# Kernel tuning notes

Hardware: AMD Instinct MI355X
Metric: run time of the kernel (lower is better)

## Reference

```python
import jax, jax.numpy as jnp
import numpy as np

EPS = 1e-8
ACT_BITS = 8


def _ternary_vq(t):
    gamma = jnp.abs(t).mean()
    q = jnp.clip(jnp.round(t / (gamma + EPS)), -1.0, 1.0)
    return q * gamma


def setup_inputs() -> dict:
    key = jax.random.key(0)
    k1, k2, k3 = jax.random.split(key, 3)
    in_features, out_features = 1024, 1024
    x = jax.random.normal(k1, (8, 4096, in_features), dtype=jnp.float32)
    weight = jax.random.normal(k2, (out_features, in_features), dtype=jnp.float32)
    bias = jax.random.normal(k3, (out_features,), dtype=jnp.float32)
    return {"x": x, "weight": weight, "bias": bias}


def reference(x, weight, bias):
    # Weight/bias ternary quantization (done once in __init__ of the module)
    wq = _ternary_vq(weight)   # [out, in]
    bq = _ternary_vq(bias)     # [out]

    # Activation quantization: power-of-two scale from global absmax
    qmax = jnp.float32(2 ** (ACT_BITS - 1) - 1)  # 127
    max_val = jnp.max(jnp.abs(x))
    scale = jnp.exp2(jnp.floor(jnp.log2(max_val / qmax + EPS)))
    xq = jnp.round(jnp.clip(x, -qmax * scale, qmax * scale) / scale) * scale

    # F.linear: x @ W^T + b
    return jnp.einsum('bsi,oi->bso', xq, wq) + bq
```

## Files before the change

kernel.cpp:

```cpp
#include <hip/hip_runtime.h>

typedef __attribute__((ext_vector_type(4))) int int4v;

constexpr int Mdim = 32768;
constexpr int Kdim = 1024;
constexpr int Ndim = 1024;
constexpr float FEPS = 1e-8f;

constexpr size_t WQ_OFF = 32768;
constexpr size_t WS_NEED = WQ_OFF + (size_t)Ndim * Kdim;

__global__ void k_pre(const uint4* __restrict__ xv, const float4* __restrict__ wv,
                      unsigned* __restrict__ pmax, float* __restrict__ partials) {
  const int tid = threadIdx.x;
  if (blockIdx.x < 2048) {
    int i0 = blockIdx.x * 256 + tid;
    const int stride = 2048 * 256;
    const int n4 = Mdim * Kdim / 4;
    unsigned m = 0u;
    for (int i = i0; i < n4; i += stride) {
      uint4 v = xv[i];
      m = max(m, v.x & 0x7fffffffu);
      m = max(m, v.y & 0x7fffffffu);
      m = max(m, v.z & 0x7fffffffu);
      m = max(m, v.w & 0x7fffffffu);
    }
    #pragma unroll
    for (int off = 32; off > 0; off >>= 1)
      m = max(m, (unsigned)__shfl_down((int)m, off, 64));
    __shared__ unsigned red[4];
    if ((tid & 63) == 0) red[tid >> 6] = m;
    __syncthreads();
    if (tid == 0)
      pmax[blockIdx.x] = max(max(red[0], red[1]), max(red[2], red[3]));
  } else {
    int wb = blockIdx.x - 2048;
    float s = 0.f;
    const int stride = 256 * 256;
    const int n4 = Ndim * Kdim / 4;
    for (int i = wb * 256 + tid; i < n4; i += stride) {
      float4 v = wv[i];
      s += fabsf(v.x) + fabsf(v.y) + fabsf(v.z) + fabsf(v.w);
    }
    __shared__ float red[256];
    red[tid] = s;
    __syncthreads();
    for (int h = 128; h > 0; h >>= 1) {
      if (tid < h) red[tid] += red[tid + h];
      __syncthreads();
    }
    if (tid == 0) partials[wb] = red[0];
  }
}

__global__ void k_finalize2(const float* __restrict__ bias, const float* __restrict__ w,
                            const float* __restrict__ partials, const unsigned* __restrict__ pmax,
                            float* __restrict__ scalars, float* __restrict__ bq,
                            unsigned char* __restrict__ wq) {
  __shared__ float red[256];
  const int t = threadIdx.x;
  const int b = blockIdx.x;

  red[t] = partials[t];
  __syncthreads();
  for (int h = 128; h > 0; h >>= 1) {
    if (t < h) red[t] += red[t + h];
    __syncthreads();
  }
  const float gw = red[0] / (1024.0f * 1024.0f);
  __syncthreads();
  const float inv_g = gw + FEPS;

  {
    const int tile = b * 4 + (t >> 6);
    const int nb = tile >> 4;
    const int kt = tile & 15;
    const int l = t & 63;
    const float4* src = (const float4*)(w + (size_t)(nb * 16 + (l >> 2)) * Kdim + kt * 64 + (l & 3) * 16);
    unsigned o[4];
    #pragma unroll
    for (int v = 0; v < 4; ++v) {
      float4 f = src[v];
      int a  = (int)rintf(fminf(fmaxf(f.x / inv_g, -1.f), 1.f));
      int bb = (int)rintf(fminf(fmaxf(f.y / inv_g, -1.f), 1.f));
      int cc = (int)rintf(fminf(fmaxf(f.z / inv_g, -1.f), 1.f));
      int dd = (int)rintf(fminf(fmaxf(f.w / inv_g, -1.f), 1.f));
      o[v] = (unsigned)(a & 0xff) | ((unsigned)(bb & 0xff) << 8) |
             ((unsigned)(cc & 0xff) << 16) | ((unsigned)(dd & 0xff) << 24);
    }
    uint4 pk; pk.x = o[0]; pk.y = o[1]; pk.z = o[2]; pk.w = o[3];
    const int lp = (l >> 2) | ((l & 3) << 4);
    *(uint4*)(wq + (size_t)tile * 1024 + lp * 16) = pk;
  }

  if (b != 0) return;

  __shared__ unsigned redu[256];
  __shared__ float sh_gb;
  unsigned m = 0u;
  #pragma unroll
  for (int i = 0; i < 8; ++i) m = max(m, pmax[t + 256 * i]);
  redu[t] = m;
  float s = fabsf(bias[t]) + fabsf(bias[t + 256]) + fabsf(bias[t + 512]) + fabsf(bias[t + 768]);
  red[t] = s;
  __syncthreads();
  for (int h = 128; h > 0; h >>= 1) {
    if (t < h) {
      red[t] += red[t + h];
      redu[t] = max(redu[t], redu[t + h]);
    }
    __syncthreads();
  }
  if (t == 0) {
    float gb = red[0] / 1024.0f;
    float maxval = __uint_as_float(redu[0]);
    float v = maxval / 127.0f + FEPS;
    int e = (int)((__float_as_uint(v) >> 23) & 0xff) - 127;
    float scale = ldexpf(1.0f, e);
    scalars[0] = gw;
    scalars[1] = gb;
    scalars[2] = scale;
    scalars[3] = scale * gw;
    scalars[4] = 127.0f * scale;
    scalars[5] = ldexpf(1.0f, -e);
    sh_gb = gb;
  }
  __syncthreads();
  float gb = sh_gb;
  for (int i = t; i < 1024; i += 256) {
    float q = rintf(bias[i] / (gb + FEPS));
    q = fminf(fmaxf(q, -1.0f), 1.0f);
    bq[i] = q * gb;
  }
}

__launch_bounds__(1024)
__global__ void k_megagemm(const float* __restrict__ x, const unsigned char* __restrict__ wq,
                           const float* __restrict__ scalars, const float* __restrict__ bq,
                           float* __restrict__ out) {
  __shared__ __align__(16) unsigned char Alds[131072];

  const int tid = threadIdx.x;
  const int lane = tid & 63;
  const int wv = tid >> 6;
  const int mtile = blockIdx.x;
  const float qs = scalars[4], inv = scalars[5];

  #pragma unroll
  for (int i = 0; i < 8; ++i) {
    const int tile = wv * 8 + i;
    const int mb = tile >> 4;
    const int kt = tile & 15;
    const float4* src = (const float4*)(x + (size_t)(mtile * 128 + mb * 16 + (lane >> 2)) * Kdim
                                          + kt * 64 + (lane & 3) * 16);
    unsigned o[4];
    #pragma unroll
    for (int v = 0; v < 4; ++v) {
      float4 f = src[v];
      int a = (int)rintf(fminf(fmaxf(f.x, -qs), qs) * inv);
      int b = (int)rintf(fminf(fmaxf(f.y, -qs), qs) * inv);
      int c = (int)rintf(fminf(fmaxf(f.z, -qs), qs) * inv);
      int d = (int)rintf(fminf(fmaxf(f.w, -qs), qs) * inv);
      o[v] = (unsigned)(a & 0xff) | ((unsigned)(b & 0xff) << 8) |
             ((unsigned)(c & 0xff) << 16) | ((unsigned)(d & 0xff) << 24);
    }
    uint4 pk; pk.x = o[0]; pk.y = o[1]; pk.z = o[2]; pk.w = o[3];
    const int lp = (lane >> 2) | ((lane & 3) << 4);
    *(uint4*)(Alds + (size_t)tile * 1024 + lp * 16) = pk;
  }
  __syncthreads();

  const int wr = wv >> 2;
  const int wc = wv & 3;
  const float sg = scalars[3];
  const unsigned char* Alds_a0 = Alds + (size_t)(wr * 2) * 16 * 1024 + lane * 16;
  const unsigned char* Alds_a1 = Alds + (size_t)(wr * 2 + 1) * 16 * 1024 + lane * 16;

  for (int np = 0; np < 4; ++np) {
    int4v acc[2][4];
    #pragma unroll
    for (int i = 0; i < 2; ++i)
      #pragma unroll
      for (int j = 0; j < 4; ++j)
        acc[i][j] = (int4v){0, 0, 0, 0};

    const unsigned char* Bb = wq + ((size_t)(np * 16 + wc * 4) * 16) * 1024 + lane * 16;

    #pragma unroll
    for (int kt = 0; kt < 16; ++kt) {
      int4v b0 = *(const int4v*)(Bb + (size_t)(0 * 16 + kt) * 1024);
      int4v b1 = *(const int4v*)(Bb + (size_t)(1 * 16 + kt) * 1024);
      int4v b2 = *(const int4v*)(Bb + (size_t)(2 * 16 + kt) * 1024);
      int4v b3 = *(const int4v*)(Bb + (size_t)(3 * 16 + kt) * 1024);
      int4v a0 = *(const int4v*)(Alds_a0 + (size_t)kt * 1024);
      int4v a1 = *(const int4v*)(Alds_a1 + (size_t)kt * 1024);
      acc[0][0] = __builtin_amdgcn_mfma_i32_16x16x64_i8(a0, b0, acc[0][0], 0, 0, 0);
      acc[0][1] = __builtin_amdgcn_mfma_i32_16x16x64_i8(a0, b1, acc[0][1], 0, 0, 0);
      acc[0][2] = __builtin_amdgcn_mfma_i32_16x16x64_i8(a0, b2, acc[0][2], 0, 0, 0);
      acc[0][3] = __builtin_amdgcn_mfma_i32_16x16x64_i8(a0, b3, acc[0][3], 0, 0, 0);
      acc[1][0] = __builtin_amdgcn_mfma_i32_16x16x64_i8(a1, b0, acc[1][0], 0, 0, 0);
      acc[1][1] = __builtin_amdgcn_mfma_i32_16x16x64_i8(a1, b1, acc[1][1], 0, 0, 0);
      acc[1][2] = __builtin_amdgcn_mfma_i32_16x16x64_i8(a1, b2, acc[1][2], 0, 0, 0);
      acc[1][3] = __builtin_amdgcn_mfma_i32_16x16x64_i8(a1, b3, acc[1][3], 0, 0, 0);
    }

    #pragma unroll
    for (int ni = 0; ni < 4; ++ni) {
      const int col = np * 256 + wc * 64 + ni * 16 + (lane & 15);
      const float bb = bq[col];
      #pragma unroll
      for (int mi = 0; mi < 2; ++mi) {
        const int rowb = mtile * 128 + wr * 32 + mi * 16 + (lane >> 4) * 4;
        #pragma unroll
        for (int r = 0; r < 4; ++r)
          out[(size_t)(rowb + r) * Ndim + col] = (float)acc[mi][ni][r] * sg + bb;
      }
    }
  }
}

extern "C" void kernel_launch(void* const* d_in, const int* in_sizes, int n_in,
                              void* d_out, int out_size, void* d_ws, size_t ws_size,
                              hipStream_t stream) {
  const float* x = (const float*)d_in[0];
  const float* weight = (const float*)d_in[1];
  const float* bias = (const float*)d_in[2];
  float* out = (float*)d_out;

  if (ws_size < WS_NEED) return;

  char* ws = (char*)d_ws;
  float* scalars = (float*)ws;
  float* partials = (float*)(ws + 1024);
  unsigned* pmax = (unsigned*)(ws + 4096);
  float* bq = (float*)(ws + 16384);
  unsigned char* wq = (unsigned char*)(ws + WQ_OFF);

  k_pre<<<2304, 256, 0, stream>>>((const uint4*)x, (const float4*)weight, pmax, partials);
  k_finalize2<<<256, 256, 0, stream>>>(bias, weight, partials, pmax, scalars, bq, wq);
  k_megagemm<<<256, 1024, 0, stream>>>(x, wq, scalars, bq, out);
}
```

Baseline: 95.94 us.

## Stage quantized weight tiles into LDS via async double-buffered loads

```diff
diff --git a/kernel.cpp b/kernel.cpp
--- a/kernel.cpp
+++ b/kernel.cpp
@@ -9,6 +9,12 @@
 
 constexpr size_t WQ_OFF = 32768;
 constexpr size_t WS_NEED = WQ_OFF + (size_t)Ndim * Kdim;
+
+__device__ __forceinline__ void gload16(const void* g, void* l) {
+  __builtin_amdgcn_global_load_lds(
+      (const __attribute__((address_space(1))) unsigned int*)g,
+      (__attribute__((address_space(3))) unsigned int*)l, 16, 0, 0);
+}
 
 __global__ void k_pre(const uint4* __restrict__ xv, const float4* __restrict__ wv,
                       unsigned* __restrict__ pmax, float* __restrict__ partials) {
@@ -134,11 +140,13 @@
   }
 }
 
-__launch_bounds__(1024)
+__launch_bounds__(512, 4)
 __global__ void k_megagemm(const float* __restrict__ x, const unsigned char* __restrict__ wq,
                            const float* __restrict__ scalars, const float* __restrict__ bq,
                            float* __restrict__ out) {
-  __shared__ __align__(16) unsigned char Alds[131072];
+  __shared__ __align__(16) unsigned char lds[81920];
+  unsigned char* Alds = lds;
+  unsigned char* Bbuf = lds + 65536;
 
   const int tid = threadIdx.x;
   const int lane = tid & 63;
@@ -151,7 +159,7 @@
     const int tile = wv * 8 + i;
     const int mb = tile >> 4;
     const int kt = tile & 15;
-    const float4* src = (const float4*)(x + (size_t)(mtile * 128 + mb * 16 + (lane >> 2)) * Kdim
+    const float4* src = (const float4*)(x + (size_t)(mtile * 64 + mb * 16 + (lane >> 2)) * Kdim
                                           + kt * 64 + (lane & 3) * 16);
     unsigned o[4];
     #pragma unroll
@@ -173,50 +181,63 @@
   const int wr = wv >> 2;
   const int wc = wv & 3;
   const float sg = scalars[3];
-  const unsigned char* Alds_a0 = Alds + (size_t)(wr * 2) * 16 * 1024 + lane * 16;
-  const unsigned char* Alds_a1 = Alds + (size_t)(wr * 2 + 1) * 16 * 1024 + lane * 16;
-
-  for (int np = 0; np < 4; ++np) {
-    int4v acc[2][4];
+  const unsigned char* A0 = Alds + ((size_t)(wr * 2 + 0) * 16) * 1024 + lane * 16;
+  const unsigned char* A1 = Alds + ((size_t)(wr * 2 + 1) * 16) * 1024 + lane * 16;
+
+#define STAGEB(np_, kt_) \
+    gload16(wq + ((size_t)(((np_) * 8 + wv) * 16 + (kt_))) * 1024 + lane * 16, \
+            Bbuf + (((kt_) & 1) * 8192) + wv * 1024 + lane * 16)
+
+  STAGEB(0, 0);
+
+  #pragma unroll 1
+  for (int np = 0; np < 8; ++np) {
+    int4v acc[2][2];
     #pragma unroll
     for (int i = 0; i < 2; ++i)
       #pragma unroll
-      for (int j = 0; j < 4; ++j)
+      for (int j = 0; j < 2; ++j)
         acc[i][j] = (int4v){0, 0, 0, 0};
 
-    const unsigned char* Bb = wq + ((size_t)(np * 16 + wc * 4) * 16) * 1024 + lane * 16;
-
     #pragma unroll
     for (int kt = 0; kt < 16; ++kt) {
-      int4v b0 = *(const int4v*)(Bb + (size_t)(0 * 16 + kt) * 1024);
-      int4v b1 = *(const int4v*)(Bb + (size_t)(1 * 16 + kt) * 1024);
-      int4v b2 = *(const int4v*)(Bb + (size_t)(2 * 16 + kt) * 1024);
-      int4v b3 = *(const int4v*)(Bb + (size_t)(3 * 16 + kt) * 1024);
-      int4v a0 = *(const int4v*)(Alds_a0 + (size_t)kt * 1024);
-      int4v a1 = *(const int4v*)(Alds_a1 + (size_t)kt * 1024);
+      if (kt == 0) {
+        if (np == 0) { asm volatile("s_waitcnt vmcnt(0)" ::: "memory"); }
+        else         { asm volatile("s_waitcnt vmcnt(16)" ::: "memory"); }
+      } else         { asm volatile("s_waitcnt vmcnt(0)" ::: "memory"); }
+      __builtin_amdgcn_s_barrier();
+      asm volatile("" ::: "memory");
+
+      if (kt < 15) { STAGEB(np, kt + 1); }
+      else if (np < 7) { STAGEB(np + 1, 0); }
+
+      const unsigned char* bb = Bbuf + ((kt & 1) * 8192) + (size_t)(wc * 2) * 1024 + lane * 16;
+      int4v b0 = *(const int4v*)(bb);
+      int4v b1 = *(const int4v*)(bb + 1024);
+      int4v a0 = *(const int4v*)(A0 + (size_t)kt * 1024);
+      int4v a1 = *(const int4v*)(A1 + (size_t)kt * 1024);
+      __builtin_amdgcn_s_setprio(1);
       acc[0][0] = __builtin_amdgcn_mfma_i32_16x16x64_i8(a0, b0, acc[0][0], 0, 0, 0);
       acc[0][1] = __builtin_amdgcn_mfma_i32_16x16x64_i8(a0, b1, acc[0][1], 0, 0, 0);
-      acc[0][2] = __builtin_amdgcn_mfma_i32_16x16x64_i8(a0, b2, acc[0][2], 0, 0, 0);
-      acc[0][3] = __builtin_amdgcn_mfma_i32_16x16x64_i8(a0, b3, acc[0][3], 0, 0, 0);
       acc[1][0] = __builtin_amdgcn_mfma_i32_16x16x64_i8(a1, b0, acc[1][0], 0, 0, 0);
       acc[1][1] = __builtin_amdgcn_mfma_i32_16x16x64_i8(a1, b1, acc[1][1], 0, 0, 0);
-      acc[1][2] = __builtin_amdgcn_mfma_i32_16x16x64_i8(a1, b2, acc[1][2], 0, 0, 0);
-      acc[1][3] = __builtin_amdgcn_mfma_i32_16x16x64_i8(a1, b3, acc[1][3], 0, 0, 0);
-    }
-
-    #pragma unroll
-    for (int ni = 0; ni < 4; ++ni) {
-      const int col = np * 256 + wc * 64 + ni * 16 + (lane & 15);
+      __builtin_amdgcn_s_setprio(0);
+    }
+
+    #pragma unroll
+    for (int nj = 0; nj < 2; ++nj) {
+      const int col = np * 128 + (wc * 2 + nj) * 16 + (lane & 15);
       const float bb = bq[col];
       #pragma unroll
       for (int mi = 0; mi < 2; ++mi) {
-        const int rowb = mtile * 128 + wr * 32 + mi * 16 + (lane >> 4) * 4;
+        const int rowb = mtile * 64 + wr * 32 + mi * 16 + (lane >> 4) * 4;
         #pragma unroll
         for (int r = 0; r < 4; ++r)
-          out[(size_t)(rowb + r) * Ndim + col] = (float)acc[mi][ni][r] * sg + bb;
+          out[(size_t)(rowb + r) * Ndim + col] = (float)acc[mi][nj][r] * sg + bb;
       }
     }
   }
+#undef STAGEB
 }
 
 extern "C" void kernel_launch(void* const* d_in, const int* in_sizes, int n_in,
@@ -238,5 +259,5 @@
 
   k_pre<<<2304, 256, 0, stream>>>((const uint4*)x, (const float4*)weight, pmax, partials);
   k_finalize2<<<256, 256, 0, stream>>>(bias, weight, partials, pmax, scalars, bq, wq);
-  k_megagemm<<<256, 1024, 0, stream>>>(x, wq, scalars, bq, out);
-}
+  k_megagemm<<<512, 512, 0, stream>>>(x, wq, scalars, bq, out);
+}
```

New measurement: 102.9 us. +7.2%, slower.

## Shrink GEMM blocks to 32-row tiles and software-pipeline B loads

Applied to the files above, without the earlier changes.

```diff
diff --git a/kernel.cpp b/kernel.cpp
--- a/kernel.cpp
+++ b/kernel.cpp
@@ -134,11 +134,11 @@
   }
 }
 
-__launch_bounds__(1024)
+__launch_bounds__(256, 4)
 __global__ void k_megagemm(const float* __restrict__ x, const unsigned char* __restrict__ wq,
                            const float* __restrict__ scalars, const float* __restrict__ bq,
                            float* __restrict__ out) {
-  __shared__ __align__(16) unsigned char Alds[131072];
+  __shared__ __align__(16) unsigned char Alds[32768];
 
   const int tid = threadIdx.x;
   const int lane = tid & 63;
@@ -151,7 +151,7 @@
     const int tile = wv * 8 + i;
     const int mb = tile >> 4;
     const int kt = tile & 15;
-    const float4* src = (const float4*)(x + (size_t)(mtile * 128 + mb * 16 + (lane >> 2)) * Kdim
+    const float4* src = (const float4*)(x + (size_t)(mtile * 32 + mb * 16 + (lane >> 2)) * Kdim
                                           + kt * 64 + (lane & 3) * 16);
     unsigned o[4];
     #pragma unroll
@@ -170,12 +170,29 @@
   }
   __syncthreads();
 
-  const int wr = wv >> 2;
-  const int wc = wv & 3;
   const float sg = scalars[3];
-  const unsigned char* Alds_a0 = Alds + (size_t)(wr * 2) * 16 * 1024 + lane * 16;
-  const unsigned char* Alds_a1 = Alds + (size_t)(wr * 2 + 1) * 16 * 1024 + lane * 16;
-
+  const unsigned char* A0 = Alds + lane * 16;
+  const unsigned char* A1 = Alds + 16 * 1024 + lane * 16;
+
+#define LB(r0, r1, r2, r3, Bb, kt_) do {                         \
+    r0 = *(const int4v*)((Bb) + (size_t)((0 * 16 + (kt_))) * 1024); \
+    r1 = *(const int4v*)((Bb) + (size_t)((1 * 16 + (kt_))) * 1024); \
+    r2 = *(const int4v*)((Bb) + (size_t)((2 * 16 + (kt_))) * 1024); \
+    r3 = *(const int4v*)((Bb) + (size_t)((3 * 16 + (kt_))) * 1024); \
+  } while (0)
+
+#define MF8(A0v, A1v, B0, B1, B2, B3) do {                                         \
+    acc[0][0] = __builtin_amdgcn_mfma_i32_16x16x64_i8(A0v, B0, acc[0][0], 0, 0, 0); \
+    acc[0][1] = __builtin_amdgcn_mfma_i32_16x16x64_i8(A0v, B1, acc[0][1], 0, 0, 0); \
+    acc[0][2] = __builtin_amdgcn_mfma_i32_16x16x64_i8(A0v, B2, acc[0][2], 0, 0, 0); \
+    acc[0][3] = __builtin_amdgcn_mfma_i32_16x16x64_i8(A0v, B3, acc[0][3], 0, 0, 0); \
+    acc[1][0] = __builtin_amdgcn_mfma_i32_16x16x64_i8(A1v, B0, acc[1][0], 0, 0, 0); \
+    acc[1][1] = __builtin_amdgcn_mfma_i32_16x16x64_i8(A1v, B1, acc[1][1], 0, 0, 0); \
+    acc[1][2] = __builtin_amdgcn_mfma_i32_16x16x64_i8(A1v, B2, acc[1][2], 0, 0, 0); \
+    acc[1][3] = __builtin_amdgcn_mfma_i32_16x16x64_i8(A1v, B3, acc[1][3], 0, 0, 0); \
+  } while (0)
+
+  #pragma unroll 1
   for (int np = 0; np < 4; ++np) {
     int4v acc[2][4];
     #pragma unroll
@@ -184,39 +201,39 @@
       for (int j = 0; j < 4; ++j)
         acc[i][j] = (int4v){0, 0, 0, 0};
 
-    const unsigned char* Bb = wq + ((size_t)(np * 16 + wc * 4) * 16) * 1024 + lane * 16;
-
-    #pragma unroll
-    for (int kt = 0; kt < 16; ++kt) {
-      int4v b0 = *(const int4v*)(Bb + (size_t)(0 * 16 + kt) * 1024);
-      int4v b1 = *(const int4v*)(Bb + (size_t)(1 * 16 + kt) * 1024);
-      int4v b2 = *(const int4v*)(Bb + (size_t)(2 * 16 + kt) * 1024);
-      int4v b3 = *(const int4v*)(Bb + (size_t)(3 * 16 + kt) * 1024);
-      int4v a0 = *(const int4v*)(Alds_a0 + (size_t)kt * 1024);
-      int4v a1 = *(const int4v*)(Alds_a1 + (size_t)kt * 1024);
-      acc[0][0] = __builtin_amdgcn_mfma_i32_16x16x64_i8(a0, b0, acc[0][0], 0, 0, 0);
-      acc[0][1] = __builtin_amdgcn_mfma_i32_16x16x64_i8(a0, b1, acc[0][1], 0, 0, 0);
-      acc[0][2] = __builtin_amdgcn_mfma_i32_16x16x64_i8(a0, b2, acc[0][2], 0, 0, 0);
-      acc[0][3] = __builtin_amdgcn_mfma_i32_16x16x64_i8(a0, b3, acc[0][3], 0, 0, 0);
-      acc[1][0] = __builtin_amdgcn_mfma_i32_16x16x64_i8(a1, b0, acc[1][0], 0, 0, 0);
-      acc[1][1] = __builtin_amdgcn_mfma_i32_16x16x64_i8(a1, b1, acc[1][1], 0, 0, 0);
-      acc[1][2] = __builtin_amdgcn_mfma_i32_16x16x64_i8(a1, b2, acc[1][2], 0, 0, 0);
-      acc[1][3] = __builtin_amdgcn_mfma_i32_16x16x64_i8(a1, b3, acc[1][3], 0, 0, 0);
-    }
-
-    #pragma unroll
-    for (int ni = 0; ni < 4; ++ni) {
-      const int col = np * 256 + wc * 64 + ni * 16 + (lane & 15);
+    const unsigned char* Bb = wq + ((size_t)(np * 16 + wv * 4) * 16) * 1024 + lane * 16;
+
+    int4v pb0, pb1, pb2, pb3, qb0, qb1, qb2, qb3;
+    LB(pb0, pb1, pb2, pb3, Bb, 0);
+    LB(qb0, qb1, qb2, qb3, Bb, 1);
+
+    #pragma unroll
+    for (int kt = 0; kt < 16; kt += 2) {
+      int4v a0 = *(const int4v*)(A0 + (size_t)kt * 1024);
+      int4v a1 = *(const int4v*)(A1 + (size_t)kt * 1024);
+      MF8(a0, a1, pb0, pb1, pb2, pb3);
+      if (kt + 2 < 16) LB(pb0, pb1, pb2, pb3, Bb, kt + 2);
+      int4v a2 = *(const int4v*)(A0 + (size_t)(kt + 1) * 1024);
+      int4v a3 = *(const int4v*)(A1 + (size_t)(kt + 1) * 1024);
+      MF8(a2, a3, qb0, qb1, qb2, qb3);
+      if (kt + 3 < 16) LB(qb0, qb1, qb2, qb3, Bb, kt + 3);
+    }
+
+    #pragma unroll
+    for (int nj = 0; nj < 4; ++nj) {
+      const int col = np * 256 + wv * 64 + nj * 16 + (lane & 15);
       const float bb = bq[col];
       #pragma unroll
       for (int mi = 0; mi < 2; ++mi) {
-        const int rowb = mtile * 128 + wr * 32 + mi * 16 + (lane >> 4) * 4;
+        const int rowb = mtile * 32 + mi * 16 + (lane >> 4) * 4;
         #pragma unroll
         for (int r = 0; r < 4; ++r)
-          out[(size_t)(rowb + r) * Ndim + col] = (float)acc[mi][ni][r] * sg + bb;
+          out[(size_t)(rowb + r) * Ndim + col] = (float)acc[mi][nj][r] * sg + bb;
       }
     }
   }
+#undef LB
+#undef MF8
 }
 
 extern "C" void kernel_launch(void* const* d_in, const int* in_sizes, int n_in,
@@ -238,5 +255,5 @@
 
   k_pre<<<2304, 256, 0, stream>>>((const uint4*)x, (const float4*)weight, pmax, partials);
   k_finalize2<<<256, 256, 0, stream>>>(bias, weight, partials, pmax, scalars, bq, wq);
-  k_megagemm<<<256, 1024, 0, stream>>>(x, wq, scalars, bq, out);
-}
+  k_megagemm<<<1024, 256, 0, stream>>>(x, wq, scalars, bq, out);
+}
```

After: 177.2 us. 84.7% more time.

## Overlap activation quantization with first N-panel MFMA compute in megagemm

Applied to the files above, without the earlier changes.

```diff
diff --git a/kernel.cpp b/kernel.cpp
--- a/kernel.cpp
+++ b/kernel.cpp
@@ -134,6 +134,15 @@
   }
 }
 
+__device__ __forceinline__ unsigned pack4q(float4 f, float qs, float inv) {
+  int a = (int)rintf(fminf(fmaxf(f.x, -qs), qs) * inv);
+  int b = (int)rintf(fminf(fmaxf(f.y, -qs), qs) * inv);
+  int c = (int)rintf(fminf(fmaxf(f.z, -qs), qs) * inv);
+  int d = (int)rintf(fminf(fmaxf(f.w, -qs), qs) * inv);
+  return (unsigned)(a & 0xff) | ((unsigned)(b & 0xff) << 8) |
+         ((unsigned)(c & 0xff) << 16) | ((unsigned)(d & 0xff) << 24);
+}
+
 __launch_bounds__(1024)
 __global__ void k_megagemm(const float* __restrict__ x, const unsigned char* __restrict__ wq,
                            const float* __restrict__ scalars, const float* __restrict__ bq,
@@ -145,78 +154,138 @@
   const int wv = tid >> 6;
   const int mtile = blockIdx.x;
   const float qs = scalars[4], inv = scalars[5];
-
-  #pragma unroll
-  for (int i = 0; i < 8; ++i) {
-    const int tile = wv * 8 + i;
-    const int mb = tile >> 4;
-    const int kt = tile & 15;
-    const float4* src = (const float4*)(x + (size_t)(mtile * 128 + mb * 16 + (lane >> 2)) * Kdim
-                                          + kt * 64 + (lane & 3) * 16);
-    unsigned o[4];
-    #pragma unroll
-    for (int v = 0; v < 4; ++v) {
-      float4 f = src[v];
-      int a = (int)rintf(fminf(fmaxf(f.x, -qs), qs) * inv);
-      int b = (int)rintf(fminf(fmaxf(f.y, -qs), qs) * inv);
-      int c = (int)rintf(fminf(fmaxf(f.z, -qs), qs) * inv);
-      int d = (int)rintf(fminf(fmaxf(f.w, -qs), qs) * inv);
-      o[v] = (unsigned)(a & 0xff) | ((unsigned)(b & 0xff) << 8) |
-             ((unsigned)(c & 0xff) << 16) | ((unsigned)(d & 0xff) << 24);
-    }
-    uint4 pk; pk.x = o[0]; pk.y = o[1]; pk.z = o[2]; pk.w = o[3];
-    const int lp = (lane >> 2) | ((lane & 3) << 4);
-    *(uint4*)(Alds + (size_t)tile * 1024 + lp * 16) = pk;
-  }
-  __syncthreads();
+  const float sg = scalars[3];
+  const int lp = (lane >> 2) | ((lane & 3) << 4);
+
+  const int qmb = wv >> 1;
+  const int qk0 = (wv & 1) * 2;
+  const float* qsrc = x + (size_t)(mtile * 128 + qmb * 16 + (lane >> 2)) * Kdim + (lane & 3) * 16;
 
   const int wr = wv >> 2;
   const int wc = wv & 3;
-  const float sg = scalars[3];
-  const unsigned char* Alds_a0 = Alds + (size_t)(wr * 2) * 16 * 1024 + lane * 16;
-  const unsigned char* Alds_a1 = Alds + (size_t)(wr * 2 + 1) * 16 * 1024 + lane * 16;
-
-  for (int np = 0; np < 4; ++np) {
+  const unsigned char* A0 = Alds + (size_t)(wr * 2) * 16 * 1024 + lane * 16;
+  const unsigned char* A1 = Alds + (size_t)(wr * 2 + 1) * 16 * 1024 + lane * 16;
+
+#define QLOAD(r0, r1, r2, r3, ktt) do {                       \
+    const float4* s_ = (const float4*)(qsrc + (ktt) * 64);    \
+    r0 = s_[0]; r1 = s_[1]; r2 = s_[2]; r3 = s_[3];           \
+  } while (0)
+
+#define QSTORE(r0, r1, r2, r3, ktt) do {                                   \
+    uint4 pk_;                                                             \
+    pk_.x = pack4q(r0, qs, inv); pk_.y = pack4q(r1, qs, inv);              \
+    pk_.z = pack4q(r2, qs, inv); pk_.w = pack4q(r3, qs, inv);              \
+    *(uint4*)(Alds + (size_t)(qmb * 16 + (ktt)) * 1024 + lp * 16) = pk_;   \
+  } while (0)
+
+#define COMPUTE_KT(Bb_, ktt) do {                                                   \
+    int4v b0 = *(const int4v*)((Bb_) + (size_t)(0 * 16 + (ktt)) * 1024);            \
+    int4v b1 = *(const int4v*)((Bb_) + (size_t)(1 * 16 + (ktt)) * 1024);            \
+    int4v b2 = *(const int4v*)((Bb_) + (size_t)(2 * 16 + (ktt)) * 1024);            \
+    int4v b3 = *(const int4v*)((Bb_) + (size_t)(3 * 16 + (ktt)) * 1024);            \
+    int4v a0 = *(const int4v*)(A0 + (size_t)(ktt) * 1024);                          \
+    int4v a1 = *(const int4v*)(A1 + (size_t)(ktt) * 1024);                          \
+    __builtin_amdgcn_s_setprio(1);                                                  \
+    acc[0][0] = __builtin_amdgcn_mfma_i32_16x16x64_i8(a0, b0, acc[0][0], 0, 0, 0);  \
+    acc[0][1] = __builtin_amdgcn_mfma_i32_16x16x64_i8(a0, b1, acc[0][1], 0, 0, 0);  \
+    acc[0][2] = __builtin_amdgcn_mfma_i32_16x16x64_i8(a0, b2, acc[0][2], 0, 0, 0);  \
+    acc[0][3] = __builtin_amdgcn_mfma_i32_16x16x64_i8(a0, b3, acc[0][3], 0, 0, 0);  \
+    acc[1][0] = __builtin_amdgcn_mfma_i32_16x16x64_i8(a1, b0, acc[1][0], 0, 0, 0);  \
+    acc[1][1] = __builtin_amdgcn_mfma_i32_16x16x64_i8(a1, b1, acc[1][1], 0, 0, 0);  \
+    acc[1][2] = __builtin_amdgcn_mfma_i32_16x16x64_i8(a1, b2, acc[1][2], 0, 0, 0);  \
+    acc[1][3] = __builtin_amdgcn_mfma_i32_16x16x64_i8(a1, b3, acc[1][3], 0, 0, 0);  \
+    __builtin_amdgcn_s_setprio(0);                                                  \
+  } while (0)
+
+#define EPILOGUE(np_) do {                                                          \
+    _Pragma("unroll")                                                               \
+    for (int nj = 0; nj < 4; ++nj) {                                                \
+      const int col = (np_) * 256 + wc * 64 + nj * 16 + (lane & 15);                \
+      const float bb = bq[col];                                                     \
+      _Pragma("unroll")                                                             \
+      for (int mi = 0; mi < 2; ++mi) {                                              \
+        const int rowb = mtile * 128 + wr * 64 + mi * 32 + (lane >> 4) * 4;         \
+        _Pragma("unroll")                                                           \
+        for (int r = 0; r < 4; ++r)                                                 \
+          out[(size_t)(rowb + r) * Ndim + col] = (float)acc[mi][nj][r] * sg + bb;   \
+      }                                                                             \
+    }                                                                               \
+  } while (0)
+
+#undef EPILOGUE
+#define EPILOGUE(np_) do {                                                          \
+    _Pragma("unroll")                                                               \
+    for (int nj = 0; nj < 4; ++nj) {                                                \
+      const int col = (np_) * 256 + wc * 64 + nj * 16 + (lane & 15);                \
+      const float bb = bq[col];                                                     \
+      _Pragma("unroll")                                                             \
+      for (int mi = 0; mi < 2; ++mi) {                                              \
+        const int rowb = mtile * 128 + (wr * 2 + mi) * 16 + (lane >> 4) * 4;        \
+        _Pragma("unroll")                                                           \
+        for (int r = 0; r < 4; ++r)                                                 \
+          out[(size_t)(rowb + r) * Ndim + col] = (float)acc[mi][nj][r] * sg + bb;   \
+      }                                                                             \
+    }                                                                               \
+  } while (0)
+
+  {
+    float4 r0, r1, r2, r3;
+    QLOAD(r0, r1, r2, r3, qk0);
+    QSTORE(r0, r1, r2, r3, qk0);
+    QLOAD(r0, r1, r2, r3, qk0 + 1);
+    QSTORE(r0, r1, r2, r3, qk0 + 1);
+  }
+  __syncthreads();
+
+  {
     int4v acc[2][4];
     #pragma unroll
     for (int i = 0; i < 2; ++i)
       #pragma unroll
       for (int j = 0; j < 4; ++j)
         acc[i][j] = (int4v){0, 0, 0, 0};
-
+    const unsigned char* Bb = wq + ((size_t)(0 * 16 + wc * 4) * 16) * 1024 + lane * 16;
+
+    #pragma unroll
+    for (int c = 0; c < 4; ++c) {
+      float4 t0a, t0b, t0c, t0d;
+      const int nk = 4 * (c + 1) + qk0;
+      if (c < 3) QLOAD(t0a, t0b, t0c, t0d, nk);
+      COMPUTE_KT(Bb, 4 * c + 0);
+      COMPUTE_KT(Bb, 4 * c + 1);
+      float4 t1a, t1b, t1c, t1d;
+      if (c < 3) {
+        QSTORE(t0a, t0b, t0c, t0d, nk);
+        QLOAD(t1a, t1b, t1c, t1d, nk + 1);
+      }
+      COMPUTE_KT(Bb, 4 * c + 2);
+      COMPUTE_KT(Bb, 4 * c + 3);
+      if (c < 3) {
+        QSTORE(t1a, t1b, t1c, t1d, nk + 1);
+        __syncthreads();
+      }
+    }
+    EPILOGUE(0);
+  }
+
+  #pragma unroll 1
+  for (int np = 1; np < 4; ++np) {
+    int4v acc[2][4];
+    #pragma unroll
+    for (int i = 0; i < 2; ++i)
+      #pragma unroll
+      for (int j = 0; j < 4; ++j)
+        acc[i][j] = (int4v){0, 0, 0, 0};
     const unsigned char* Bb = wq + ((size_t)(np * 16 + wc * 4) * 16) * 1024 + lane * 16;
-
-    #pragma unroll
-    for (int kt = 0; kt < 16; ++kt) {
-      int4v b0 = *(const int4v*)(Bb + (size_t)(0 * 16 + kt) * 1024);
-      int4v b1 = *(const int4v*)(Bb + (size_t)(1 * 16 + kt) * 1024);
-      int4v b2 = *(const int4v*)(Bb + (size_t)(2 * 16 + kt) * 1024);
-      int4v b3 = *(const int4v*)(Bb + (size_t)(3 * 16 + kt) * 1024);
-      int4v a0 = *(const int4v*)(Alds_a0 + (size_t)kt * 1024);
-      int4v a1 = *(const int4v*)(Alds_a1 + (size_t)kt * 1024);
-      acc[0][0] = __builtin_amdgcn_mfma_i32_16x16x64_i8(a0, b0, acc[0][0], 0, 0, 0);
-      acc[0][1] = __builtin_amdgcn_mfma_i32_16x16x64_i8(a0, b1, acc[0][1], 0, 0, 0);
-      acc[0][2] = __builtin_amdgcn_mfma_i32_16x16x64_i8(a0, b2, acc[0][2], 0, 0, 0);
-      acc[0][3] = __builtin_amdgcn_mfma_i32_16x16x64_i8(a0, b3, acc[0][3], 0, 0, 0);
-      acc[1][0] = __builtin_amdgcn_mfma_i32_16x16x64_i8(a1, b0, acc[1][0], 0, 0, 0);
-      acc[1][1] = __builtin_amdgcn_mfma_i32_16x16x64_i8(a1, b1, acc[1][1], 0, 0, 0);
-      acc[1][2] = __builtin_amdgcn_mfma_i32_16x16x64_i8(a1, b2, acc[1][2], 0, 0, 0);
-      acc[1][3] = __builtin_amdgcn_mfma_i32_16x16x64_i8(a1, b3, acc[1][3], 0, 0, 0);
-    }
-
-    #pragma unroll
-    for (int ni = 0; ni < 4; ++ni) {
-      const int col = np * 256 + wc * 64 + ni * 16 + (lane & 15);
-      const float bb = bq[col];
-      #pragma unroll
-      for (int mi = 0; mi < 2; ++mi) {
-        const int rowb = mtile * 128 + wr * 32 + mi * 16 + (lane >> 4) * 4;
-        #pragma unroll
-        for (int r = 0; r < 4; ++r)
-          out[(size_t)(rowb + r) * Ndim + col] = (float)acc[mi][ni][r] * sg + bb;
-      }
-    }
-  }
+    #pragma unroll
+    for (int kt = 0; kt < 16; ++kt)
+      COMPUTE_KT(Bb, kt);
+    EPILOGUE(np);
+  }
+#undef QLOAD
+#undef QSTORE
+#undef COMPUTE_KT
+#undef EPILOGUE
 }
 
 extern "C" void kernel_launch(void* const* d_in, const int* in_sizes, int n_in,
```

New measurement: 175.5 us. 83.0% more time.
